# Optimization experiments

Hardware: AMD Instinct MI355X
Metric: run time of the kernel (lower is better)

The kernel has to match this reference:

```python
import jax, jax.numpy as jnp
import numpy as np
from functools import partial

F_DIM, DETER, STOCH, HEADS = 1024, 256, 1024, 8
HD = F_DIM // HEADS  # 128
LN_EPS = 1e-5


def _layer_norm(x, g, b):
    m = jnp.mean(x, axis=-1, keepdims=True)
    v = jnp.var(x, axis=-1, keepdims=True)
    return (x - m) * jax.lax.rsqrt(v + LN_EPS) * g + b


def _forward(emb_vision, emb_text, emb_proprio, noise, h0, s0,
             proj_vision_w, proj_vision_b, proj_text_w, proj_text_b,
             proj_proprio_w, proj_proprio_b,
             attn_in_w, attn_in_b, attn_out_w, attn_out_b, importance,
             fuse_w1, fuse_b1, fuse_w2, fuse_b2, ln_g, ln_b,
             gru_w_ih, gru_w_hh, gru_b_ih, gru_b_hh,
             prior_w, prior_b, post_w, post_b):
    B, T = emb_vision.shape[:2]
    N = B * T
    # --- multimodal fusion, vectorized over all (B,T) steps ---
    pv = emb_vision @ proj_vision_w.T + proj_vision_b      # (B,T,F)
    pt = emb_text @ proj_text_w.T + proj_text_b
    pp = emb_proprio @ proj_proprio_w.T + proj_proprio_b
    stacked = jnp.stack([pv, pt, pp], axis=2).reshape(N, 3, F_DIM)  # (N,3,F)
    # self-attention over the 3 modality tokens (nn.MultiheadAttention)
    qkv = stacked @ attn_in_w.T + attn_in_b                 # (N,3,3F)
    q, k, v = jnp.split(qkv, 3, axis=-1)
    q = q.reshape(N, 3, HEADS, HD)
    k = k.reshape(N, 3, HEADS, HD)
    v = v.reshape(N, 3, HEADS, HD)
    scores = jnp.einsum('nqhd,nkhd->nhqk', q, k) / jnp.sqrt(jnp.float32(HD))
    attn = jax.nn.softmax(scores, axis=-1)
    att = jnp.einsum('nhqk,nkhd->nqhd', attn, v).reshape(N, 3, F_DIM)
    att = att @ attn_out_w.T + attn_out_b
    imp = jax.nn.softmax(importance)
    weighted = att * imp[None, :, None]
    concat = weighted.reshape(N, 3 * F_DIM)
    fused = jax.nn.relu(concat @ fuse_w1.T + fuse_b1) @ fuse_w2.T + fuse_b2
    fused = _layer_norm(fused, ln_g, ln_b).reshape(B, T, F_DIM)

    # --- sequential RSSM rollout ---
    def step(carry, xt):
        h, s = carry
        f_t, n_t = xt
        x = jnp.concatenate([s, f_t], axis=-1)              # (B, 2048)
        gi = x @ gru_w_ih.T + gru_b_ih                      # (B, 3*DETER)
        gh = h @ gru_w_hh.T + gru_b_hh
        ir, iz, inn = jnp.split(gi, 3, axis=-1)
        hr, hz, hn = jnp.split(gh, 3, axis=-1)
        r = jax.nn.sigmoid(ir + hr)
        z = jax.nn.sigmoid(iz + hz)
        n = jnp.tanh(inn + r * hn)
        h_new = (1.0 - z) * n + z * h
        prior = h_new @ prior_w.T + prior_b                 # (B, STOCH)
        post = jnp.concatenate([h_new, f_t], -1) @ post_w.T + post_b
        s_new = post + n_t                                  # reparameterized sample (unit std)
        out = jnp.concatenate([h_new, s_new, prior, post], axis=-1)
        return (h_new, s_new), out

    fused_T = jnp.swapaxes(fused, 0, 1)                     # (T,B,F)
    noise_T = jnp.swapaxes(noise, 0, 1)
    _, outs = jax.lax.scan(step, (h0, s0), (fused_T, noise_T))
    return jnp.swapaxes(outs, 0, 1)                         # (B,T,256+1024+1024+1024)


def setup_inputs() -> dict:
    key = jax.random.key(0)
    ks = iter(jax.random.split(key, 40))
    B, T = 64, 128

    def w(shape):
        fan_in = shape[-1]
        return jax.random.normal(next(ks), shape, jnp.float32) / np.sqrt(fan_in)

    d = {
        'emb_vision': jax.random.normal(next(ks), (B, T, 512), jnp.float32),
        'emb_text': jax.random.normal(next(ks), (B, T, 512), jnp.float32),
        'emb_proprio': jax.random.normal(next(ks), (B, T, 256), jnp.float32),
        'noise': jax.random.normal(next(ks), (B, T, STOCH), jnp.float32),
        'h0': jnp.zeros((B, DETER), jnp.float32),
        's0': jnp.zeros((B, STOCH), jnp.float32),
        'proj_vision_w': w((F_DIM, 512)), 'proj_vision_b': jnp.zeros((F_DIM,), jnp.float32),
        'proj_text_w': w((F_DIM, 512)), 'proj_text_b': jnp.zeros((F_DIM,), jnp.float32),
        'proj_proprio_w': w((F_DIM, 256)), 'proj_proprio_b': jnp.zeros((F_DIM,), jnp.float32),
        'attn_in_w': w((3 * F_DIM, F_DIM)), 'attn_in_b': jnp.zeros((3 * F_DIM,), jnp.float32),
        'attn_out_w': w((F_DIM, F_DIM)), 'attn_out_b': jnp.zeros((F_DIM,), jnp.float32),
        'importance': jnp.ones((3,), jnp.float32),
        'fuse_w1': w((F_DIM, 3 * F_DIM)), 'fuse_b1': jnp.zeros((F_DIM,), jnp.float32),
        'fuse_w2': w((F_DIM, F_DIM)), 'fuse_b2': jnp.zeros((F_DIM,), jnp.float32),
        'ln_g': jnp.ones((F_DIM,), jnp.float32), 'ln_b': jnp.zeros((F_DIM,), jnp.float32),
        'gru_w_ih': w((3 * DETER, F_DIM + STOCH)), 'gru_w_hh': w((3 * DETER, DETER)),
        'gru_b_ih': jnp.zeros((3 * DETER,), jnp.float32), 'gru_b_hh': jnp.zeros((3 * DETER,), jnp.float32),
        'prior_w': w((STOCH, DETER)), 'prior_b': jnp.zeros((STOCH,), jnp.float32),
        'post_w': w((STOCH, DETER + F_DIM)), 'post_b': jnp.zeros((STOCH,), jnp.float32),
    }
    return d


def reference(emb_vision, emb_text, emb_proprio, noise, h0, s0,
              proj_vision_w, proj_vision_b, proj_text_w, proj_text_b,
              proj_proprio_w, proj_proprio_b,
              attn_in_w, attn_in_b, attn_out_w, attn_out_b, importance,
              fuse_w1, fuse_b1, fuse_w2, fuse_b2, ln_g, ln_b,
              gru_w_ih, gru_w_hh, gru_b_ih, gru_b_hh,
              prior_w, prior_b, post_w, post_b):
    return _forward(emb_vision, emb_text, emb_proprio, noise, h0, s0,
                    proj_vision_w, proj_vision_b, proj_text_w, proj_text_b,
                    proj_proprio_w, proj_proprio_b,
                    attn_in_w, attn_in_b, attn_out_w, attn_out_b, importance,
                    fuse_w1, fuse_b1, fuse_w2, fuse_b2, ln_g, ln_b,
                    gru_w_ih, gru_w_hh, gru_b_ih, gru_b_hh,
                    prior_w, prior_b, post_w, post_b)
```

## Files before the change

kernel.cpp:

```cpp
#include <hip/hip_runtime.h>
#include <cstdint>
#include <cstddef>

#define F4(p)  (*(reinterpret_cast<float4*>(p)))
#define CF4(p) (*(reinterpret_cast<const float4*>(p)))

typedef __attribute__((ext_vector_type(8))) short short8;
typedef __attribute__((ext_vector_type(4))) float f32x4;
typedef __attribute__((ext_vector_type(4))) int i32x4;

__device__ __forceinline__ float bf2f(unsigned short h) {
  return __uint_as_float(((unsigned int)h) << 16);
}
__device__ __forceinline__ unsigned short f2bf(float x) {
  unsigned int u = __float_as_uint(x);
  return (unsigned short)((u + 0x7FFFu + ((u >> 16) & 1u)) >> 16);
}

#if __has_builtin(__builtin_amdgcn_global_load_lds)
#define USE_GLL 1
#else
#define USE_GLL 0
#endif
#if __has_builtin(__builtin_amdgcn_sched_barrier)
#define SCHED_BARRIER() __builtin_amdgcn_sched_barrier(0)
#else
#define SCHED_BARRIER()
#endif

__device__ __forceinline__ void stage16(unsigned short* lds_lane,
                                        unsigned short* lds_wavebase,
                                        const unsigned short* g) {
#if USE_GLL
  __builtin_amdgcn_global_load_lds(
      (const __attribute__((address_space(1))) unsigned int*)g,
      (__attribute__((address_space(3))) unsigned int*)lds_wavebase, 16, 0, 0);
#else
  *(short8*)lds_lane = *(const short8*)g;
#endif
}

__device__ __forceinline__ i32x4 coh_load16(const void* p) {
  i32x4 r;
  asm volatile("global_load_dwordx4 %0, %1, off sc0 sc1"
               : "=v"(r) : "v"(p) : "memory");
  return r;
}
__device__ __forceinline__ void coh_store16(void* p, i32x4 v) {
  asm volatile("global_store_dwordx4 %0, %1, off sc0 sc1"
               :: "v"(p), "v"(v) : "memory");
}

__device__ __forceinline__ float fsigmoid(float x) {
  return 1.0f / (1.0f + __expf(-x));
}
__device__ __forceinline__ float ftanh(float x) {
  float ax = fabsf(x);
  float e = __expf(2.0f * ax);
  float t = 1.0f - 2.0f / (e + 1.0f);
  return copysignf(t, x);
}

__global__ __launch_bounds__(256) void gemm_bf(
    const unsigned short* __restrict__ A, int lda,
    const unsigned short* __restrict__ A2, int lda2, int kSplit,
    const unsigned short* __restrict__ B, int ldb,
    const unsigned short* __restrict__ B2, int ldb2, int nSplit,
    void* __restrict__ Cv, int ldc, int K,
    const float* __restrict__ bias,
    const float* __restrict__ src, int ldsrc, int src_c0,
    const float* __restrict__ scale_ptr, int relu, int obf16, int qperm)
{
  __shared__ unsigned short As[128 * 64];
  __shared__ unsigned short Bs[128 * 64];
  const int tid = threadIdx.x;
  const int wv = tid >> 6, ln = tid & 63;
  const int wm = wv >> 1, wn = wv & 1;
  const size_t gm0 = (size_t)blockIdx.y * 128;
  const size_t gn0 = (size_t)blockIdx.x * 128;

  f32x4 acc[4][4];
  #pragma unroll
  for (int i = 0; i < 4; ++i)
    #pragma unroll
    for (int j = 0; j < 4; ++j) acc[i][j] = (f32x4){0.f, 0.f, 0.f, 0.f};

  for (int kk = 0; kk < K; kk += 64) {
    const unsigned short* Ause = A; int lduse = lda; int kkA = kk;
    if (A2 != nullptr && kk >= kSplit) { Ause = A2; lduse = lda2; kkA = kk - kSplit; }
    #pragma unroll
    for (int j = 0; j < 4; ++j) {
      int idx = j * 256 + tid;
      int r = idx >> 3, u = idx & 7;
      int ksw = (u ^ (r & 7)) << 3;
      const unsigned short* ga = Ause + (gm0 + r) * lduse + kkA + ksw;
      stage16(&As[idx * 8], &As[(idx & ~63) * 8], ga);
      size_t nr = gn0 + r;
      const unsigned short* gb = (nr < (size_t)nSplit)
          ? B + nr * ldb + kk + ksw
          : B2 + (nr - nSplit) * ldb2 + kk + ksw;
      stage16(&Bs[idx * 8], &Bs[(idx & ~63) * 8], gb);
    }
    __syncthreads();
    #pragma unroll
    for (int ks = 0; ks < 2; ++ks) {
      short8 af[4], bfv[4];
      #pragma unroll
      for (int mi = 0; mi < 4; ++mi) {
        int r = wm * 64 + mi * 16 + (ln & 15);
        int u = (ks * 4 + (ln >> 4)) ^ (r & 7);
        af[mi] = *(const short8*)&As[(r * 8 + u) * 8];
      }
      #pragma unroll
      for (int nj = 0; nj < 4; ++nj) {
        int r = wn * 64 + nj * 16 + (ln & 15);
        int u = (ks * 4 + (ln >> 4)) ^ (r & 7);
        bfv[nj] = *(const short8*)&Bs[(r * 8 + u) * 8];
      }
      #pragma unroll
      for (int mi = 0; mi < 4; ++mi)
        #pragma unroll
        for (int nj = 0; nj < 4; ++nj)
          acc[mi][nj] = __builtin_amdgcn_mfma_f32_16x16x32_bf16(
              af[mi], bfv[nj], acc[mi][nj], 0, 0, 0);
    }
    __syncthreads();
  }

  float sc = scale_ptr ? *scale_ptr : 1.0f;
  #pragma unroll
  for (int nj = 0; nj < 4; ++nj) {
    int gc = (int)gn0 + wn * 64 + nj * 16 + (ln & 15);
    float bv = bias ? bias[gc] : 0.f;
    #pragma unroll
    for (int mi = 0; mi < 4; ++mi) {
      #pragma unroll
      for (int qq = 0; qq < 4; ++qq) {
        int gr = (int)gm0 + wm * 64 + mi * 16 + ((ln >> 4) << 2) + qq;
        float v = acc[mi][nj][qq] * sc + bv;
        if (src && gc >= src_c0) v += src[(size_t)gr * ldsrc + (gc - src_c0)];
        if (relu) v = fmaxf(v, 0.f);
        if (qperm) {
          int t = gr & 127, bq = gr >> 7;
          int g = gc >> 8, d = gc & 255;
          int ddq = d >> 5, doff = d & 31;
          int wq = bq >> 4;
          int lq = (bq & 15) + ((doff >> 3) << 4);
          size_t qi = (((((size_t)t * 8 + ddq) * 3 + g) * 4 + wq) * 64 + lq) * 8
                      + (doff & 7);
          ((float*)Cv)[qi] = v;
        } else if (obf16) {
          ((unsigned short*)Cv)[(size_t)gr * ldc + gc] = f2bf(v);
        } else {
          ((float*)Cv)[(size_t)gr * ldc + gc] = v;
        }
      }
    }
  }
}

__global__ __launch_bounds__(256) void cvt_bf(
    const float* __restrict__ in, unsigned short* __restrict__ outp, int n4)
{
  int i = blockIdx.x * 256 + threadIdx.x;
  if (i < n4) {
    float4 v = CF4(in + (size_t)i * 4);
    ushort4 o;
    o.x = f2bf(v.x); o.y = f2bf(v.y); o.z = f2bf(v.z); o.w = f2bf(v.w);
    *(ushort4*)(outp + (size_t)i * 4) = o;
  }
}

__global__ __launch_bounds__(256) void transpose_bf(
    const float* __restrict__ in, int ldin, unsigned short* __restrict__ outp, int R)
{
  __shared__ float tile[32][33];
  int c0 = blockIdx.x * 32, r0 = blockIdx.y * 32;
  int tx = threadIdx.x & 31, ty = threadIdx.x >> 5;
  #pragma unroll
  for (int i = ty; i < 32; i += 8)
    tile[i][tx] = in[(size_t)(r0 + i) * ldin + c0 + tx];
  __syncthreads();
  #pragma unroll
  for (int i = ty; i < 32; i += 8)
    outp[(size_t)(c0 + i) * R + r0 + tx] = f2bf(tile[tx][i]);
}

__global__ __launch_bounds__(64) void matvec3(
    const float* __restrict__ A,
    const float* __restrict__ x0, const float* __restrict__ x1,
    const float* __restrict__ x2, const float* __restrict__ aib,
    float* __restrict__ outp)
{
  int i = blockIdx.x, t = threadIdx.x;
  const float* Ar = A + (size_t)i * 1024;
  float s0 = 0.f, s1 = 0.f, s2 = 0.f;
  for (int k = t * 4; k < 1024; k += 256) {
    float4 a = CF4(Ar + k);
    float4 v0 = CF4(x0 + k), v1 = CF4(x1 + k), v2 = CF4(x2 + k);
    s0 += a.x*v0.x + a.y*v0.y + a.z*v0.z + a.w*v0.w;
    s1 += a.x*v1.x + a.y*v1.y + a.z*v1.z + a.w*v1.w;
    s2 += a.x*v2.x + a.y*v2.y + a.z*v2.z + a.w*v2.w;
  }
  #pragma unroll
  for (int m = 32; m > 0; m >>= 1) {
    s0 += __shfl_xor(s0, m); s1 += __shfl_xor(s1, m); s2 += __shfl_xor(s2, m);
  }
  if (t == 0) {
    float b = aib[i];
    outp[i] = s0 + b; outp[3072 + i] = s1 + b; outp[6144 + i] = s2 + b;
  }
}

__global__ __launch_bounds__(64) void matvec_nt(
    const float* __restrict__ A, int lda,
    const float* __restrict__ x, const float* __restrict__ badd,
    float* __restrict__ outp, int K)
{
  int i = blockIdx.x, t = threadIdx.x;
  const float* Ar = A + (size_t)i * lda;
  float s = 0.f;
  for (int k = t * 4; k < K; k += 256) {
    float4 a = CF4(Ar + k);
    float4 xx = CF4(x + k);
    s += a.x*xx.x + a.y*xx.y + a.z*xx.z + a.w*xx.w;
  }
  #pragma unroll
  for (int m = 32; m > 0; m >>= 1) s += __shfl_xor(s, m);
  if (t == 0) outp[i] = s + (badd ? badd[i] : 0.f);
}

__global__ __launch_bounds__(256) void imp_rep_k(
    const float* __restrict__ importance, const float* __restrict__ aob,
    float* __restrict__ imp, float* __restrict__ rep)
{
  __shared__ float si[3];
  if (threadIdx.x == 0) {
    float a = importance[0], b = importance[1], c = importance[2];
    float mx = fmaxf(a, fmaxf(b, c));
    float ea = expf(a - mx), eb = expf(b - mx), ec = expf(c - mx);
    float inv = 1.f / (ea + eb + ec);
    si[0] = ea * inv; si[1] = eb * inv; si[2] = ec * inv;
    imp[0] = si[0]; imp[1] = si[1]; imp[2] = si[2];
  }
  __syncthreads();
  for (int idx = threadIdx.x; idx < 3072; idx += 256)
    rep[idx] = si[idx >> 10] * aob[idx & 1023];
}

__global__ __launch_bounds__(256) void bias_prep(
    const float* __restrict__ gbih, const float* __restrict__ gbhh,
    const float* __restrict__ prb, float* __restrict__ cb768,
    float* __restrict__ cb2048)
{
  int i = blockIdx.x * 256 + threadIdx.x;
  if (i < 768) cb768[i] = gbih[i] + (i < 512 ? gbhh[i] : 0.f);
  if (i < 2048) cb2048[i] = (i < 1024) ? prb[i] : 0.f;
}

__global__ __launch_bounds__(256) void attn3(
    const unsigned short* __restrict__ qkv, unsigned short* __restrict__ att)
{
  const int n = blockIdx.x;
  const unsigned short* row = qkv + (size_t)n * 9216;
  __shared__ float qk[6144];
  __shared__ float sc[72];
  __shared__ float pw[72];
  const int t = threadIdx.x;
  for (int idx = t; idx < 768; idx += 256) {
    int m = idx >> 7;
    int off = (idx & 127) << 3;
    const unsigned short* srcp = (m < 3) ? (row + m * 3072 + off)
                                         : (row + (m - 3) * 3072 + 1024 + off);
    short8 v = *(const short8*)srcp;
    float* dst = &qk[m * 1024 + off];
    #pragma unroll
    for (int j = 0; j < 8; ++j) dst[j] = bf2f(((const unsigned short*)&v)[j]);
  }
  __syncthreads();
  if (t < 72) {
    int h = t / 9, i = (t % 9) / 3, j = t % 3;
    const float* qp = &qk[i * 1024 + h * 128];
    const float* kp = &qk[3072 + j * 1024 + h * 128];
    float s = 0.f;
    int rot = (t & 31) * 4;
    for (int d2 = 0; d2 < 128; ++d2) {
      int dx = (d2 + rot) & 127;
      s += qp[dx] * kp[dx];
    }
    sc[t] = s * 0.08838834764831845f;
  }
  __syncthreads();
  if (t < 24) {
    int base = t * 3;
    float a = sc[base], b = sc[base + 1], c = sc[base + 2];
    float mx = fmaxf(a, fmaxf(b, c));
    float ea = expf(a - mx), eb = expf(b - mx), ec = expf(c - mx);
    float inv = 1.f / (ea + eb + ec);
    pw[base] = ea * inv; pw[base + 1] = eb * inv; pw[base + 2] = ec * inv;
  }
  __syncthreads();
  unsigned short* outp = att + (size_t)n * 3072;
  #pragma unroll
  for (int rep = 0; rep < 3; ++rep) {
    int idx = (rep * 256 + t) << 2;
    int i = idx >> 10;
    int hd = idx & 1023;
    int h = hd >> 7;
    int pb = (h * 3 + i) * 3;
    float w0 = pw[pb], w1 = pw[pb + 1], w2 = pw[pb + 2];
    ushort4 v0 = *(const ushort4*)(row + 2048 + hd);
    ushort4 v1 = *(const ushort4*)(row + 3072 + 2048 + hd);
    ushort4 v2 = *(const ushort4*)(row + 6144 + 2048 + hd);
    ushort4 o;
    o.x = f2bf(w0 * bf2f(v0.x) + w1 * bf2f(v1.x) + w2 * bf2f(v2.x));
    o.y = f2bf(w0 * bf2f(v0.y) + w1 * bf2f(v1.y) + w2 * bf2f(v2.y));
    o.z = f2bf(w0 * bf2f(v0.z) + w1 * bf2f(v1.z) + w2 * bf2f(v2.z));
    o.w = f2bf(w0 * bf2f(v0.w) + w1 * bf2f(v1.w) + w2 * bf2f(v2.w));
    *(ushort4*)(outp + idx) = o;
  }
}

__global__ __launch_bounds__(256) void layernorm_bf(
    unsigned short* __restrict__ X, const float* __restrict__ g,
    const float* __restrict__ bta)
{
  int n = blockIdx.x, t = threadIdx.x;
  unsigned short* row = X + (size_t)n * 1024;
  ushort4 hv = *(ushort4*)(row + t * 4);
  float x0 = bf2f(hv.x), x1 = bf2f(hv.y), x2 = bf2f(hv.z), x3 = bf2f(hv.w);
  float s = x0 + x1 + x2 + x3;
  float ss = x0*x0 + x1*x1 + x2*x2 + x3*x3;
  #pragma unroll
  for (int m = 32; m > 0; m >>= 1) { s += __shfl_xor(s, m); ss += __shfl_xor(ss, m); }
  __shared__ float rs[4], rss[4];
  int w = t >> 6;
  if ((t & 63) == 0) { rs[w] = s; rss[w] = ss; }
  __syncthreads();
  s = rs[0] + rs[1] + rs[2] + rs[3];
  ss = rss[0] + rss[1] + rss[2] + rss[3];
  float mean = s * (1.0f / 1024.0f);
  float var = ss * (1.0f / 1024.0f) - mean * mean;
  float inv = 1.0f / sqrtf(var + 1e-5f);
  float4 gg = CF4(g + t * 4);
  float4 bb = CF4(bta + t * 4);
  ushort4 o;
  o.x = f2bf((x0 - mean) * inv * gg.x + bb.x);
  o.y = f2bf((x1 - mean) * inv * gg.y + bb.y);
  o.z = f2bf((x2 - mean) * inv * gg.z + bb.z);
  o.w = f2bf((x3 - mean) * inv * gg.w + bb.w);
  *(ushort4*)(row + t * 4) = o;
}

__global__ __launch_bounds__(256) void build_R_bf(
    const float* __restrict__ Fpb, const float* __restrict__ noise,
    const float* __restrict__ s0, unsigned short* __restrict__ R)
{
  size_t idx = (size_t)blockIdx.x * 256 + threadIdx.x;
  int n = (int)(idx >> 8);
  int k4 = (int)(idx & 255) << 2;
  float4 v;
  if ((n & 127) == 0) {
    v = CF4(s0 + (size_t)(n >> 7) * 1024 + k4);
  } else {
    float4 f = CF4(Fpb + (size_t)(n - 1) * 1024 + k4);
    float4 z = CF4(noise + (size_t)(n - 1) * 1024 + k4);
    v.x = f.x + z.x; v.y = f.y + z.y; v.z = f.z + z.z; v.w = f.w + z.w;
  }
  ushort4 o;
  o.x = f2bf(v.x); o.y = f2bf(v.y); o.z = f2bf(v.z); o.w = f2bf(v.w);
  *(ushort4*)(R + (size_t)n * 1024 + k4) = o;
}

__global__ __launch_bounds__(256) void s_out_k(
    float* __restrict__ outp, const float* __restrict__ noise)
{
  size_t idx = (size_t)blockIdx.x * 256 + threadIdx.x;
  int n = (int)(idx >> 8);
  int j4 = (int)(idx & 255) << 2;
  float4 p = CF4(outp + (size_t)n * 3328 + 2304 + j4);
  float4 z = CF4(noise + (size_t)n * 1024 + j4);
  float4 o; o.x = p.x + z.x; o.y = p.y + z.y; o.z = p.z + z.z; o.w = p.w + z.w;
  F4(outp + (size_t)n * 3328 + 256 + j4) = o;
}

__global__ __launch_bounds__(256) void wr_prep(
    const unsigned short* __restrict__ M1bf, const unsigned short* __restrict__ Whhbf,
    unsigned short* __restrict__ Wr)
{
  int idx = blockIdx.x * 256 + threadIdx.x;
  int j = idx & 7, l = (idx >> 3) & 63, kt = (idx >> 9) & 7;
  int rest = idx >> 12;
  int r = rest % 12, dd = rest / 12;
  int g = r >> 1, dhalf = r & 1;
  int d = dd * 32 + dhalf * 16 + (l & 15);
  int srow = (g % 3) * 256 + d;
  int k = kt * 32 + ((l >> 4) << 3) + j;
  const unsigned short* srcp = (g < 3) ? M1bf : Whhbf;
  Wr[idx] = srcp[(size_t)srow * 256 + k];
}

__global__ __launch_bounds__(256) void h0_prep(
    const float* __restrict__ h0, unsigned short* __restrict__ hist)
{
  int idx = blockIdx.x * 256 + threadIdx.x;
  int j = idx & 7, l = (idx >> 3) & 63, kt = (idx >> 9) & 7, w = idx >> 12;
  int b = 16 * w + (l & 15);
  int k = kt * 32 + ((l >> 4) << 3) + j;
  hist[idx] = f2bf(h0[(size_t)b * 256 + k]);
}

#define LOADQ(tt) do { \
  _Pragma("unroll") \
  for (int g = 0; g < 3; ++g) { \
    const float* qp = Qr + (((((size_t)(tt) * 8 + dd) * 3 + g) * 4 + w) * 64 + l) * 8; \
    float4 qa = CF4(qp); float4 qb = CF4(qp + 4); \
    qv[g][0] = qa.x; qv[g][1] = qa.y; qv[g][2] = qa.z; qv[g][3] = qa.w; \
    qv[g][4] = qb.x; qv[g][5] = qb.y; qv[g][6] = qb.z; qv[g][7] = qb.w; \
  } } while (0)

__global__ __launch_bounds__(256, 1) void rssm_recur5(
    const unsigned short* __restrict__ Wr, const float* __restrict__ Qr,
    const float* __restrict__ bhh_n, unsigned short* __restrict__ hist,
    unsigned short* __restrict__ Hrow, float* __restrict__ outp,
    unsigned int* __restrict__ counter)
{
  const int dd = blockIdx.x;
  const int tid = threadIdx.x;
  const int w = tid >> 6, l = tid & 63;
  __shared__ float G[12][16][68];
  __shared__ unsigned short hL[16384];

  short8 Bf[3][8];
  {
    const unsigned short* wb = Wr + ((size_t)(dd * 12 + w * 3) * 8) * 512 + l * 8;
    #pragma unroll
    for (int ri = 0; ri < 3; ++ri)
      #pragma unroll
      for (int kt = 0; kt < 8; ++kt)
        Bf[ri][kt] = *(const short8*)(wb + (size_t)(ri * 8 + kt) * 512);
  }
  float bhn[8];
  #pragma unroll
  for (int j = 0; j < 8; ++j) bhn[j] = bhh_n[dd * 32 + ((l >> 4) << 3) + j];

  const int bg = w * 16 + (l & 15);
  const int dhalf = l >> 5;
  const int d16b = ((l >> 4) & 1) << 3;
  float qv[3][8];
  LOADQ(0);

  unsigned int target = 0;
  #pragma unroll 1
  for (int t = 0; t < 128; ++t) {
    const unsigned short* hsrc = hist + (size_t)(t & 1) * 16384;
    i32x4 sv[8];
    #pragma unroll
    for (int j = 0; j < 8; ++j)
      sv[j] = coh_load16(hsrc + (size_t)(j * 256 + tid) * 8);
    asm volatile("s_waitcnt vmcnt(0)" ::: "memory");
    SCHED_BARRIER();
    #pragma unroll
    for (int j = 0; j < 8; ++j)
      *(i32x4*)&hL[(size_t)(j * 256 + tid) * 8] = sv[j];
    __syncthreads();

    f32x4 acc[4][3];
    #pragma unroll
    for (int bt = 0; bt < 4; ++bt)
      #pragma unroll
      for (int ri = 0; ri < 3; ++ri) acc[bt][ri] = (f32x4){0.f, 0.f, 0.f, 0.f};
    #pragma unroll
    for (int kt = 0; kt < 8; ++kt)
      #pragma unroll
      for (int bt = 0; bt < 4; ++bt) {
        short8 a = *(const short8*)&hL[((bt * 8 + kt) * 64 + l) * 8];
        acc[bt][0] = __builtin_amdgcn_mfma_f32_16x16x32_bf16(a, Bf[0][kt], acc[bt][0], 0, 0, 0);
        acc[bt][1] = __builtin_amdgcn_mfma_f32_16x16x32_bf16(a, Bf[1][kt], acc[bt][1], 0, 0, 0);
        acc[bt][2] = __builtin_amdgcn_mfma_f32_16x16x32_bf16(a, Bf[2][kt], acc[bt][2], 0, 0, 0);
      }
    short8 ha = *(const short8*)&hL[((w * 8 + dd) * 64 + l) * 8];

    #pragma unroll
    for (int bt = 0; bt < 4; ++bt)
      #pragma unroll
      for (int ri = 0; ri < 3; ++ri)
        *(f32x4*)&G[w * 3 + ri][l & 15][bt * 16 + ((l >> 4) << 2)] = acc[bt][ri];
    __syncthreads();

    const float m1s = (t == 0) ? 0.f : 1.f;
    unsigned short hn8[8];
    float hf8[8];
    #pragma unroll
    for (int j = 0; j < 8; ++j) {
      int d16 = d16b + j;
      float m1r = G[0 + dhalf][d16][bg];
      float m1z = G[2 + dhalf][d16][bg];
      float m1n = G[4 + dhalf][d16][bg];
      float ghr = G[6 + dhalf][d16][bg];
      float ghz = G[8 + dhalf][d16][bg];
      float ghn = G[10 + dhalf][d16][bg] + bhn[j];
      float gir = fmaf(m1r, m1s, qv[0][j]);
      float giz = fmaf(m1z, m1s, qv[1][j]);
      float gin = fmaf(m1n, m1s, qv[2][j]);
      float r = fsigmoid(gir + ghr);
      float z = fsigmoid(giz + ghz);
      float nn = ftanh(gin + r * ghn);
      float hold = bf2f(((const unsigned short*)&ha)[j]);
      float hn = (1.f - z) * nn + z * hold;
      unsigned short hbv = f2bf(hn);
      hn8[j] = hbv;
      hf8[j] = bf2f(hbv);
    }

    union { short8 s; i32x4 i; } hu;
    hu.s = *(const short8*)hn8;
    coh_store16(hist + (size_t)((t + 1) & 1) * 16384
                + (size_t)((w * 8 + dd) * 64 + l) * 8, hu.i);

    if (t < 127) {
      asm volatile("s_waitcnt vmcnt(0)" ::: "memory");
      __syncthreads();
      target += 8;
      if (tid == 0)
        __hip_atomic_fetch_add(counter, 1u, __ATOMIC_RELAXED,
                               __HIP_MEMORY_SCOPE_AGENT);
      LOADQ(t + 1);
      *(short8*)(Hrow + (size_t)(bg * 128 + t) * 256 + dd * 32 + ((l >> 4) << 3)) =
          *(const short8*)hn8;
      float* op = outp + (size_t)(bg * 128 + t) * 3328 + dd * 32 + ((l >> 4) << 3);
      float4 o0; o0.x = hf8[0]; o0.y = hf8[1]; o0.z = hf8[2]; o0.w = hf8[3];
      float4 o1; o1.x = hf8[4]; o1.y = hf8[5]; o1.z = hf8[6]; o1.w = hf8[7];
      F4(op) = o0; F4(op + 4) = o1;
      if (tid == 0) {
        while (__hip_atomic_load(counter, __ATOMIC_RELAXED,
                                 __HIP_MEMORY_SCOPE_AGENT) < target) {}
      }
      __syncthreads();
    } else {
      *(short8*)(Hrow + (size_t)(bg * 128 + t) * 256 + dd * 32 + ((l >> 4) << 3)) =
          *(const short8*)hn8;
      float* op = outp + (size_t)(bg * 128 + t) * 3328 + dd * 32 + ((l >> 4) << 3);
      float4 o0; o0.x = hf8[0]; o0.y = hf8[1]; o0.z = hf8[2]; o0.w = hf8[3];
      float4 o1; o1.x = hf8[4]; o1.y = hf8[5]; o1.z = hf8[6]; o1.w = hf8[7];
      F4(op) = o0; F4(op + 4) = o1;
    }
  }
}

static inline void g_bf(const unsigned short* A, int lda,
                        const unsigned short* B, int ldb,
                        void* C, int ldc, int M, int N, int K,
                        const float* bias, const float* src, int ldsrc,
                        const float* scale, int relu, int obf16, hipStream_t s,
                        const unsigned short* A2 = nullptr, int lda2 = 0,
                        int kSplit = 1 << 30,
                        const unsigned short* B2 = nullptr, int ldb2 = 0,
                        int nSplit = 1 << 30,
                        int src_c0 = 0, int qperm = 0)
{
  dim3 grid(N / 128, M / 128);
  gemm_bf<<<grid, 256, 0, s>>>(A, lda, A2, lda2, kSplit, B, ldb, B2, ldb2, nSplit,
                               C, ldc, K, bias, src, ldsrc, src_c0, scale, relu,
                               obf16, qperm);
}

extern "C" void kernel_launch(void* const* d_in, const int* in_sizes, int n_in,
                              void* d_out, int out_size, void* d_ws, size_t ws_size,
                              hipStream_t stream)
{
  (void)in_sizes; (void)n_in; (void)out_size;

  const float* emb_v = (const float*)d_in[0];
  const float* emb_t = (const float*)d_in[1];
  const float* emb_p = (const float*)d_in[2];
  const float* noise = (const float*)d_in[3];
  const float* h0    = (const float*)d_in[4];
  const float* s0    = (const float*)d_in[5];
  const float* pvw   = (const float*)d_in[6];
  const float* pvb   = (const float*)d_in[7];
  const float* ptw   = (const float*)d_in[8];
  const float* ptb   = (const float*)d_in[9];
  const float* ppw   = (const float*)d_in[10];
  const float* ppb   = (const float*)d_in[11];
  const float* aiw   = (const float*)d_in[12];
  const float* aib   = (const float*)d_in[13];
  const float* aow   = (const float*)d_in[14];
  const float* aob   = (const float*)d_in[15];
  const float* importance = (const float*)d_in[16];
  const float* fw1   = (const float*)d_in[17];
  const float* fb1   = (const float*)d_in[18];
  const float* fw2   = (const float*)d_in[19];
  const float* fb2   = (const float*)d_in[20];
  const float* ln_g  = (const float*)d_in[21];
  const float* ln_b  = (const float*)d_in[22];
  const float* gwih  = (const float*)d_in[23];
  const float* gwhh  = (const float*)d_in[24];
  const float* gbih  = (const float*)d_in[25];
  const float* gbhh  = (const float*)d_in[26];
  const float* prw   = (const float*)d_in[27];
  const float* prb   = (const float*)d_in[28];
  const float* pow_  = (const float*)d_in[29];
  const float* pob   = (const float*)d_in[30];

  float* out = (float*)d_out;
  char* W = (char*)d_ws;

  size_t off = 0;
  auto alloc = [&](size_t bytes) { off = (off + 63) & ~63ull; size_t o = off; off += bytes; return o; };
  const size_t o_cnt    = alloc(256);
  const size_t o_imp    = alloc(16);
  const size_t o_rep    = alloc(3072 * 4);
  const size_t o_bqkv   = alloc(9216 * 4);
  const size_t o_bf1    = alloc(1024 * 4);
  const size_t o_cb768  = alloc(768 * 4);
  const size_t o_cb2048 = alloc(2048 * 4);
  const size_t o_gwihb  = alloc(768ull * 2048 * 2);
  const size_t o_whhb   = alloc(768ull * 256 * 2);
  const size_t o_m1b    = alloc(768ull * 256 * 2);
  const size_t o_prwb   = alloc(1024ull * 256 * 2);
  const size_t o_powb   = alloc(1024ull * 1280 * 2);
  const size_t o_wr     = alloc(393216ull * 2);
  const size_t o_hist   = alloc(2ull * 16384 * 2);
  const size_t o_hrow   = alloc(8192ull * 256 * 2);
  const size_t o_fusedb = alloc(8192ull * 1024 * 2);
  const size_t o_fpb    = alloc(8192ull * 1024 * 4);
  const size_t o_rbf    = alloc(8192ull * 1024 * 2);
  const size_t o_embvb  = alloc(8192ull * 512 * 2);
  const size_t o_embtb  = alloc(8192ull * 512 * 2);
  const size_t o_embpb  = alloc(8192ull * 256 * 2);
  const size_t o_wqv    = alloc(3072ull * 512 * 2);
  const size_t o_wqt    = alloc(3072ull * 512 * 2);
  const size_t o_wqp    = alloc(3072ull * 256 * 2);
  const size_t o_wf1    = alloc(1024ull * 3072 * 2);
  const size_t o_fw2b   = alloc(1024ull * 1024 * 2);
  const size_t o_fused1 = alloc(8192ull * 1024 * 2);
  const size_t o_sub    = (off + 63) & ~63ull;

  const size_t so_aiwb = 0;
  const size_t so_fw1b = so_aiwb + 3072ull * 1024 * 2;
  const size_t so_pTv  = so_fw1b + 1024ull * 3072 * 2;
  const size_t so_pTt  = so_pTv + 512ull * 1024 * 2;
  const size_t so_pTp  = so_pTt + 512ull * 1024 * 2;
  const size_t so_aoT  = so_pTp + 256ull * 1024 * 2;
  const size_t so_WphT = so_aoT + 1024ull * 1024 * 2;
  const size_t prep_bytes = so_WphT + 256ull * 1024 * 2;
  const size_t q_bytes = 8192ull * 768 * 4;

  int NC = 512;
  for (int cand : {8192, 4096, 2048, 1024}) {
    size_t sub = prep_bytes > q_bytes ? prep_bytes : q_bytes;
    size_t cb = (size_t)cand * 9216 * 2 + (size_t)cand * 3072 * 2;
    if (cb > sub) sub = cb;
    if (o_sub + sub <= ws_size) { NC = cand; break; }
  }
  const size_t o_qkvc = o_sub;
  const size_t o_attc = o_sub + (size_t)NC * 9216 * 2;
  const size_t o_qr   = o_sub;

  auto FP = [&](size_t o) { return (float*)(W + o); };
  auto UP = [&](size_t o) { return (unsigned short*)(W + o); };

  hipMemsetAsync(W + o_cnt, 0, 256, stream);
  imp_rep_k<<<1, 256, 0, stream>>>(importance, aob, FP(o_imp), FP(o_rep));
  bias_prep<<<8, 256, 0, stream>>>(gbih, gbhh, prb, FP(o_cb768), FP(o_cb2048));

  auto cvt = [&](const float* in, unsigned short* op, size_t n) {
    int n4 = (int)(n / 4);
    cvt_bf<<<(n4 + 255) / 256, 256, 0, stream>>>(in, op, n4);
  };
  cvt(aiw,  UP(o_sub + so_aiwb), 3072ull * 1024);
  cvt(fw1,  UP(o_sub + so_fw1b), 1024ull * 3072);
  cvt(fw2,  UP(o_fw2b), 1024ull * 1024);
  cvt(gwih, UP(o_gwihb), 768ull * 2048);
  cvt(gwhh, UP(o_whhb), 768ull * 256);
  cvt(prw,  UP(o_prwb), 1024ull * 256);
  cvt(pow_, UP(o_powb), 1024ull * 1280);
  cvt(emb_v, UP(o_embvb), 8192ull * 512);
  cvt(emb_t, UP(o_embtb), 8192ull * 512);
  cvt(emb_p, UP(o_embpb), 8192ull * 256);

  transpose_bf<<<dim3(16, 32), 256, 0, stream>>>(pvw, 512, UP(o_sub + so_pTv), 1024);
  transpose_bf<<<dim3(16, 32), 256, 0, stream>>>(ptw, 512, UP(o_sub + so_pTt), 1024);
  transpose_bf<<<dim3(8, 32), 256, 0, stream>>>(ppw, 256, UP(o_sub + so_pTp), 1024);
  transpose_bf<<<dim3(32, 32), 256, 0, stream>>>(aow, 1024, UP(o_sub + so_aoT), 1024);
  transpose_bf<<<dim3(8, 32), 256, 0, stream>>>(pow_, 1280, UP(o_sub + so_WphT), 1024);

  matvec3<<<3072, 64, 0, stream>>>(aiw, pvb, ptb, ppb, aib, FP(o_bqkv));
  matvec_nt<<<1024, 64, 0, stream>>>(fw1, 3072, FP(o_rep), fb1, FP(o_bf1), 3072);

  g_bf(UP(o_sub + so_aiwb), 1024, UP(o_sub + so_pTv), 1024, UP(o_wqv), 512,
       3072, 512, 1024, nullptr, nullptr, 0, nullptr, 0, 1, stream);
  g_bf(UP(o_sub + so_aiwb), 1024, UP(o_sub + so_pTt), 1024, UP(o_wqt), 512,
       3072, 512, 1024, nullptr, nullptr, 0, nullptr, 0, 1, stream);
  g_bf(UP(o_sub + so_aiwb), 1024, UP(o_sub + so_pTp), 1024, UP(o_wqp), 256,
       3072, 256, 1024, nullptr, nullptr, 0, nullptr, 0, 1, stream);
  for (int m = 0; m < 3; ++m)
    g_bf(UP(o_sub + so_fw1b) + m * 1024, 3072, UP(o_sub + so_aoT), 1024,
         UP(o_wf1) + m * 1024, 3072, 1024, 1024, 1024,
         nullptr, nullptr, 0, FP(o_imp) + m, 0, 1, stream);
  g_bf(UP(o_gwihb), 2048, UP(o_sub + so_WphT), 1024, UP(o_m1b), 256,
       768, 256, 1024, nullptr, nullptr, 0, nullptr, 0, 1, stream);

  wr_prep<<<1536, 256, 0, stream>>>(UP(o_m1b), UP(o_whhb), UP(o_wr));
  h0_prep<<<64, 256, 0, stream>>>(h0, UP(o_hist));

  const int nchunk = 8192 / NC;
  for (int c = 0; c < nchunk; ++c) {
    g_bf(UP(o_embvb) + (size_t)c * NC * 512, 512, UP(o_wqv), 512,
         UP(o_qkvc) + 0, 9216, NC, 3072, 512, FP(o_bqkv) + 0,
         nullptr, 0, nullptr, 0, 1, stream);
    g_bf(UP(o_embtb) + (size_t)c * NC * 512, 512, UP(o_wqt), 512,
         UP(o_qkvc) + 3072, 9216, NC, 3072, 512, FP(o_bqkv) + 3072,
         nullptr, 0, nullptr, 0, 1, stream);
    g_bf(UP(o_embpb) + (size_t)c * NC * 256, 256, UP(o_wqp), 256,
         UP(o_qkvc) + 6144, 9216, NC, 3072, 256, FP(o_bqkv) + 6144,
         nullptr, 0, nullptr, 0, 1, stream);
    attn3<<<NC, 256, 0, stream>>>(UP(o_qkvc), UP(o_attc));
    g_bf(UP(o_attc), 3072, UP(o_wf1), 3072,
         UP(o_fused1) + (size_t)c * NC * 1024, 1024, NC, 1024, 3072,
         FP(o_bf1), nullptr, 0, nullptr, 1 , 1, stream);
  }

  g_bf(UP(o_fused1), 1024, UP(o_fw2b), 1024, UP(o_fusedb), 1024,
       8192, 1024, 1024, fb2, nullptr, 0, nullptr, 0, 1, stream);
  layernorm_bf<<<8192, 256, 0, stream>>>(UP(o_fusedb), ln_g, ln_b);

  g_bf(UP(o_fusedb), 1024, UP(o_powb) + 256, 1280, FP(o_fpb), 1024,
       8192, 1024, 1024, pob, nullptr, 0, nullptr, 0, 0, stream);
  build_R_bf<<<8192, 256, 0, stream>>>(FP(o_fpb), noise, s0, UP(o_rbf));
  g_bf(UP(o_rbf), 1024, UP(o_gwihb), 2048, FP(o_qr), 768,
       8192, 768, 2048, FP(o_cb768), nullptr, 0, nullptr, 0, 0, stream,
       UP(o_fusedb), 1024, 1024, nullptr, 0, 1 << 30, 0, 1 );

  rssm_recur5<<<8, 256, 0, stream>>>(UP(o_wr), FP(o_qr), gbhh + 512, UP(o_hist),
                                     UP(o_hrow), out, (unsigned int*)(W + o_cnt));

  g_bf(UP(o_hrow), 256, UP(o_prwb), 256, out + 1280, 3328,
       8192, 2048, 256, FP(o_cb2048), FP(o_fpb), 1024, nullptr, 0, 0, stream,
       nullptr, 0, 1 << 30, UP(o_powb), 1280, 1024, 1024 , 0);
  s_out_k<<<8192, 256, 0, stream>>>(out, noise);
}
```

Measured before the change: 1.454 ms.

## Pin recurrent blocks to one XCC and relax coherence bits

The recurrent kernel now launches 256 blocks, and only the first eight that land on XCC 0 claim roles through an atomic counter. The rest exit at once. Because all eight worker blocks then share one L2, the hidden-state exchange loads and stores drop the sc1 bit and keep only sc0. The goal is to cut the per-step inter-block sync and data-exchange latency across the 128 sequential steps. This relies on the role counter being reset before each call, and on at least eight blocks landing on XCC 0 and being co-resident there; otherwise blocks could deadlock.

```diff
diff --git a/kernel.cpp b/kernel.cpp
--- a/kernel.cpp
+++ b/kernel.cpp
@@ -42,12 +42,12 @@
 
 __device__ __forceinline__ i32x4 coh_load16(const void* p) {
   i32x4 r;
-  asm volatile("global_load_dwordx4 %0, %1, off sc0 sc1"
+  asm volatile("global_load_dwordx4 %0, %1, off sc0"
                : "=v"(r) : "v"(p) : "memory");
   return r;
 }
 __device__ __forceinline__ void coh_store16(void* p, i32x4 v) {
-  asm volatile("global_store_dwordx4 %0, %1, off sc0 sc1"
+  asm volatile("global_store_dwordx4 %0, %1, off sc0"
                :: "v"(p), "v"(v) : "memory");
 }
 
@@ -419,14 +419,29 @@
     qv[g][4] = qb.x; qv[g][5] = qb.y; qv[g][6] = qb.z; qv[g][7] = qb.w; \
   } } while (0)
 
-__global__ __launch_bounds__(256, 1) void rssm_recur5(
+__global__ __launch_bounds__(256, 1) void rssm_recur6(
     const unsigned short* __restrict__ Wr, const float* __restrict__ Qr,
     const float* __restrict__ bhh_n, unsigned short* __restrict__ hist,
     unsigned short* __restrict__ Hrow, float* __restrict__ outp,
-    unsigned int* __restrict__ counter)
-{
-  const int dd = blockIdx.x;
+    unsigned int* __restrict__ counters)
+{
   const int tid = threadIdx.x;
+  __shared__ int s_role;
+  if (tid == 0) {
+    unsigned int xcc;
+    asm volatile("s_getreg_b32 %0, hwreg(HW_REG_XCC_ID)" : "=s"(xcc));
+    int role = -1;
+    if ((xcc & 7u) == 0u) {
+      unsigned int r = __hip_atomic_fetch_add(&counters[8], 1u, __ATOMIC_RELAXED,
+                                              __HIP_MEMORY_SCOPE_AGENT);
+      if (r < 8u) role = (int)r;
+    }
+    s_role = role;
+  }
+  __syncthreads();
+  const int dd = s_role;
+  if (dd < 0) return;
+
   const int w = tid >> 6, l = tid & 63;
   __shared__ float G[12][16][68];
   __shared__ unsigned short hL[16384];
@@ -523,7 +538,7 @@
       __syncthreads();
       target += 8;
       if (tid == 0)
-        __hip_atomic_fetch_add(counter, 1u, __ATOMIC_RELAXED,
+        __hip_atomic_fetch_add(&counters[0], 1u, __ATOMIC_RELAXED,
                                __HIP_MEMORY_SCOPE_AGENT);
       LOADQ(t + 1);
       *(short8*)(Hrow + (size_t)(bg * 128 + t) * 256 + dd * 32 + ((l >> 4) << 3)) =
@@ -533,7 +548,7 @@
       float4 o1; o1.x = hf8[4]; o1.y = hf8[5]; o1.z = hf8[6]; o1.w = hf8[7];
       F4(op) = o0; F4(op + 4) = o1;
       if (tid == 0) {
-        while (__hip_atomic_load(counter, __ATOMIC_RELAXED,
+        while (__hip_atomic_load(&counters[0], __ATOMIC_RELAXED,
                                  __HIP_MEMORY_SCOPE_AGENT) < target) {}
       }
       __syncthreads();
@@ -733,8 +748,8 @@
        8192, 768, 2048, FP(o_cb768), nullptr, 0, nullptr, 0, 0, stream,
        UP(o_fusedb), 1024, 1024, nullptr, 0, 1 << 30, 0, 1 );
 
-  rssm_recur5<<<8, 256, 0, stream>>>(UP(o_wr), FP(o_qr), gbhh + 512, UP(o_hist),
-                                     UP(o_hrow), out, (unsigned int*)(W + o_cnt));
+  rssm_recur6<<<256, 256, 0, stream>>>(UP(o_wr), FP(o_qr), gbhh + 512, UP(o_hist),
+                                       UP(o_hrow), out, (unsigned int*)(W + o_cnt));
 
   g_bf(UP(o_hrow), 256, UP(o_prwb), 256, out + 1280, 3328,
        8192, 2048, 256, FP(o_cb2048), FP(o_fpb), 1024, nullptr, 0, 0, stream,
```

Measured after the change: 1.359 ms. 1.07x faster.
